# Performance work log

Measured on AMD Instinct MI355X. Metric: run time of the kernel, lower is better.

Reference implementation:

```python
import jax, jax.numpy as jnp
import numpy as np

VLAD_K = 8   # vlad_cluster
GHOST = 2    # ghost_cluster
EPS = 1e-12  # F.normalize eps


def setup_inputs() -> dict:
    key = jax.random.key(0)
    k1, k2, k3, k4 = jax.random.split(key, 4)
    N, C, H, W = 32, 512, 16, 32
    KG = VLAD_K + GHOST
    x = jax.random.normal(k1, (N, C, H, W), dtype=jnp.float32)
    conv_w = jax.random.normal(k2, (KG, C), dtype=jnp.float32) * 0.05  # 1x1 conv weight
    conv_b = jax.random.normal(k3, (KG,), dtype=jnp.float32) * 0.05
    centers = jax.random.uniform(k4, (KG, C), dtype=jnp.float32)
    return {"x": x, "conv_w": conv_w, "conv_b": conv_b, "centers": centers}


def _l2norm(v, axis):
    n = jnp.sqrt(jnp.sum(v * v, axis=axis, keepdims=True))
    return v / jnp.maximum(n, EPS)


def reference(x, conv_w, conv_b, centers):
    N, C, H, W = x.shape
    L = H * W
    xf = x.reshape(N, C, L)  # [N, C, HW]
    # 1x1 conv -> logits [N, K+G, HW], softmax over cluster dim
    logits = jnp.einsum('kc,ncl->nkl', conv_w, xf) + conv_b[None, :, None]
    a = jax.nn.softmax(logits, axis=1)
    # sum_l a[n,k,l]*(x[n,c,l] - centers[k,c]) decomposed into two small matmuls
    assign_x = jnp.einsum('nkl,ncl->nkc', a, xf)          # [N, K+G, C]
    assign_sum = jnp.sum(a, axis=-1)                      # [N, K+G]
    cluster_res = assign_x - assign_sum[:, :, None] * centers[None]
    cluster_res = cluster_res[:, :VLAD_K, :]              # drop ghost clusters
    cluster_res = _l2norm(cluster_res, axis=-1)           # intra-norm
    vlad = cluster_res.reshape(N, -1)                     # [N, K*C]
    return _l2norm(vlad, axis=-1)
```

## Files before the change

### kernel.cpp

```cpp
#include <hip/hip_runtime.h>

#define N_   32
#define C_   512
#define L_   512
#define KG_  10
#define K_   8
#define LCH  8
#define LT   64
#define EPSF 1e-12f

__global__ __launch_bounds__(512) void k_softmax(
    const float* __restrict__ x, const float* __restrict__ cw,
    const float* __restrict__ cb, float* __restrict__ a_out,
    float* __restrict__ asum_part)
{
    const int n   = blockIdx.x;
    const int ch  = blockIdx.y;
    const int tid = threadIdx.x;
    const int l   = tid & 63;
    const int cg  = tid >> 6;
    const int lg  = ch * LT + l;

    const float* xn = x + (size_t)n * C_ * L_;

    float acc[KG_];
#pragma unroll
    for (int k = 0; k < KG_; ++k) acc[k] = 0.f;

    const int c0 = cg * 64;
#pragma unroll 4
    for (int ci = 0; ci < 64; ++ci) {
        const int c = c0 + ci;
        const float xv = xn[(size_t)c * L_ + lg];
#pragma unroll
        for (int k = 0; k < KG_; ++k)
            acc[k] += cw[k * C_ + c] * xv;
    }

    __shared__ float red[8][LT][KG_];
#pragma unroll
    for (int k = 0; k < KG_; ++k) red[cg][l][k] = acc[k];
    __syncthreads();

    __shared__ float lgs[LT][KG_];
    for (int idx = tid; idx < LT * KG_; idx += 512) {
        const int li = idx / KG_, k = idx % KG_;
        float s = 0.f;
#pragma unroll
        for (int g = 0; g < 8; ++g) s += red[g][li][k];
        lgs[li][k] = s;
    }
    __syncthreads();

    if (tid < LT) {
        float v[KG_];
        float m = -1e30f;
#pragma unroll
        for (int k = 0; k < KG_; ++k) {
            v[k] = lgs[tid][k] + cb[k];
            m = fmaxf(m, v[k]);
        }
        float s = 0.f;
#pragma unroll
        for (int k = 0; k < KG_; ++k) { v[k] = __expf(v[k] - m); s += v[k]; }
        const float inv = 1.f / s;
        const int lgl = ch * LT + tid;
#pragma unroll
        for (int k = 0; k < K_; ++k) {
            const float av = v[k] * inv;
            a_out[((size_t)n * K_ + k) * L_ + lgl] = av;
            float t = av;
#pragma unroll
            for (int off = 32; off > 0; off >>= 1) t += __shfl_down(t, off);
            if (tid == 0)
                asum_part[((size_t)n * LCH + ch) * K_ + k] = t;
        }
    }
}

__global__ __launch_bounds__(512) void k_assign(
    const float* __restrict__ x, const float* __restrict__ a,
    float* __restrict__ assign_x)
{
    const int n   = blockIdx.x;
    const int ch  = blockIdx.y;
    const int tid = threadIdx.x;

    __shared__ float xs[C_ * 65];

    const float* xbase = x + (size_t)n * C_ * L_ + ch * LT;
    for (int it = tid; it < C_ * 16; it += 512) {
        const int c = it >> 4, q = it & 15;
        const float4 v = *reinterpret_cast<const float4*>(xbase + (size_t)c * L_ + q * 4);
        const int b = c * 65 + q * 4;
        xs[b]     = v.x;
        xs[b + 1] = v.y;
        xs[b + 2] = v.z;
        xs[b + 3] = v.w;
    }
    __syncthreads();

    const int c = tid;
    const float* arow = a + (size_t)n * K_ * L_ + ch * LT;

    float acc[K_];
#pragma unroll
    for (int k = 0; k < K_; ++k) acc[k] = 0.f;

#pragma unroll 2
    for (int li = 0; li < LT; ++li) {
        const float xv = xs[c * 65 + li];
#pragma unroll
        for (int k = 0; k < K_; ++k)
            acc[k] += arow[k * L_ + li] * xv;
    }

#pragma unroll
    for (int k = 0; k < K_; ++k)
        atomicAdd(&assign_x[((size_t)n * K_ + k) * C_ + c], acc[k]);
}

__global__ __launch_bounds__(256) void k_final(
    const float* __restrict__ assign_x, const float* __restrict__ asum_part,
    const float* __restrict__ centers, float* __restrict__ out)
{
    const int n    = blockIdx.x;
    const int tid  = threadIdx.x;
    const int lane = tid & 63;
    const int wv   = tid >> 6;

    __shared__ float s_asum[K_];
    __shared__ float s_inv[K_];
    __shared__ float s_q[K_];
    __shared__ float s_ginv;
    __shared__ float wred[4][K_];

    if (tid < K_) {
        float s = 0.f;
#pragma unroll
        for (int c2 = 0; c2 < LCH; ++c2)
            s += asum_part[((size_t)n * LCH + c2) * K_ + tid];
        s_asum[tid] = s;
    }
    __syncthreads();

    float r[K_][2];
    float ssq[K_];
#pragma unroll
    for (int k = 0; k < K_; ++k) ssq[k] = 0.f;

#pragma unroll
    for (int j = 0; j < 2; ++j) {
        const int c = tid + j * 256;
#pragma unroll
        for (int k = 0; k < K_; ++k) {
            const float v = assign_x[((size_t)n * K_ + k) * C_ + c]
                          - s_asum[k] * centers[k * C_ + c];
            r[k][j] = v;
            ssq[k] += v * v;
        }
    }

#pragma unroll
    for (int k = 0; k < K_; ++k) {
        float t = ssq[k];
#pragma unroll
        for (int off = 32; off > 0; off >>= 1) t += __shfl_down(t, off);
        if (lane == 0) wred[wv][k] = t;
    }
    __syncthreads();

    if (tid < K_) {
        const float t = wred[0][tid] + wred[1][tid] + wred[2][tid] + wred[3][tid];
        const float inv = 1.f / fmaxf(sqrtf(t), EPSF);
        s_inv[tid] = inv;
        s_q[tid]   = t * inv * inv;
    }
    __syncthreads();

    if (tid == 0) {
        float g = 0.f;
#pragma unroll
        for (int k = 0; k < K_; ++k) g += s_q[k];
        s_ginv = 1.f / fmaxf(sqrtf(g), EPSF);
    }
    __syncthreads();

    const float ginv = s_ginv;
#pragma unroll
    for (int j = 0; j < 2; ++j) {
        const int c = tid + j * 256;
#pragma unroll
        for (int k = 0; k < K_; ++k)
            out[(size_t)n * (K_ * C_) + k * C_ + c] = r[k][j] * s_inv[k] * ginv;
    }
}

extern "C" void kernel_launch(void* const* d_in, const int* in_sizes, int n_in,
                              void* d_out, int out_size, void* d_ws, size_t ws_size,
                              hipStream_t stream)
{
    const float* x       = (const float*)d_in[0];
    const float* conv_w  = (const float*)d_in[1];
    const float* conv_b  = (const float*)d_in[2];
    const float* centers = (const float*)d_in[3];
    float* out = (float*)d_out;

    float* a         = (float*)d_ws;
    float* asum_part = a + (size_t)N_ * K_ * L_;
    float* assign_x  = asum_part + (size_t)N_ * LCH * K_;

    hipMemsetAsync(assign_x, 0, sizeof(float) * N_ * K_ * C_, stream);

    dim3 grid(N_, LCH);
    hipLaunchKernelGGL(k_softmax, grid, dim3(512), 0, stream,
                       x, conv_w, conv_b, a, asum_part);
    hipLaunchKernelGGL(k_assign, grid, dim3(512), 0, stream,
                       x, a, assign_x);
    hipLaunchKernelGGL(k_final, dim3(N_), dim3(256), 0, stream,
                       assign_x, asum_part, centers, out);
}
```

Baseline: 103.8 us.

## Fuse softmax and assignment kernels, reuse staged x tile, replace atomics with partials

```diff
diff --git a/kernel.cpp b/kernel.cpp
--- a/kernel.cpp
+++ b/kernel.cpp
@@ -7,92 +7,30 @@
 #define K_   8
 #define LCH  8
 #define LT   64
+#define XP   65
+#define RP   11
 #define EPSF 1e-12f
 
-__global__ __launch_bounds__(512) void k_softmax(
+__global__ __launch_bounds__(512, 2) void k_main(
     const float* __restrict__ x, const float* __restrict__ cw,
-    const float* __restrict__ cb, float* __restrict__ a_out,
+    const float* __restrict__ cb, float* __restrict__ part,
     float* __restrict__ asum_part)
 {
+    __shared__ float xs[C_ * XP];
+    __shared__ float red[8][LT][RP];
+    __shared__ float a_s[LT][K_];
+
     const int n   = blockIdx.x;
     const int ch  = blockIdx.y;
     const int tid = threadIdx.x;
-    const int l   = tid & 63;
-    const int cg  = tid >> 6;
-    const int lg  = ch * LT + l;
-
-    const float* xn = x + (size_t)n * C_ * L_;
-
-    float acc[KG_];
-#pragma unroll
-    for (int k = 0; k < KG_; ++k) acc[k] = 0.f;
-
-    const int c0 = cg * 64;
-#pragma unroll 4
-    for (int ci = 0; ci < 64; ++ci) {
-        const int c = c0 + ci;
-        const float xv = xn[(size_t)c * L_ + lg];
-#pragma unroll
-        for (int k = 0; k < KG_; ++k)
-            acc[k] += cw[k * C_ + c] * xv;
-    }
-
-    __shared__ float red[8][LT][KG_];
-#pragma unroll
-    for (int k = 0; k < KG_; ++k) red[cg][l][k] = acc[k];
-    __syncthreads();
-
-    __shared__ float lgs[LT][KG_];
-    for (int idx = tid; idx < LT * KG_; idx += 512) {
-        const int li = idx / KG_, k = idx % KG_;
-        float s = 0.f;
-#pragma unroll
-        for (int g = 0; g < 8; ++g) s += red[g][li][k];
-        lgs[li][k] = s;
-    }
-    __syncthreads();
-
-    if (tid < LT) {
-        float v[KG_];
-        float m = -1e30f;
-#pragma unroll
-        for (int k = 0; k < KG_; ++k) {
-            v[k] = lgs[tid][k] + cb[k];
-            m = fmaxf(m, v[k]);
-        }
-        float s = 0.f;
-#pragma unroll
-        for (int k = 0; k < KG_; ++k) { v[k] = __expf(v[k] - m); s += v[k]; }
-        const float inv = 1.f / s;
-        const int lgl = ch * LT + tid;
-#pragma unroll
-        for (int k = 0; k < K_; ++k) {
-            const float av = v[k] * inv;
-            a_out[((size_t)n * K_ + k) * L_ + lgl] = av;
-            float t = av;
-#pragma unroll
-            for (int off = 32; off > 0; off >>= 1) t += __shfl_down(t, off);
-            if (tid == 0)
-                asum_part[((size_t)n * LCH + ch) * K_ + k] = t;
-        }
-    }
-}
-
-__global__ __launch_bounds__(512) void k_assign(
-    const float* __restrict__ x, const float* __restrict__ a,
-    float* __restrict__ assign_x)
-{
-    const int n   = blockIdx.x;
-    const int ch  = blockIdx.y;
-    const int tid = threadIdx.x;
-
-    __shared__ float xs[C_ * 65];
 
     const float* xbase = x + (size_t)n * C_ * L_ + ch * LT;
-    for (int it = tid; it < C_ * 16; it += 512) {
+#pragma unroll
+    for (int j = 0; j < 16; ++j) {
+        const int it = tid + j * 512;
         const int c = it >> 4, q = it & 15;
         const float4 v = *reinterpret_cast<const float4*>(xbase + (size_t)c * L_ + q * 4);
-        const int b = c * 65 + q * 4;
+        const int b = c * XP + q * 4;
         xs[b]     = v.x;
         xs[b + 1] = v.y;
         xs[b + 2] = v.z;
@@ -100,28 +38,96 @@
     }
     __syncthreads();
 
+    const int l  = tid & 63;
+    const int cg = tid >> 6;
+    const int c0 = __builtin_amdgcn_readfirstlane(cg) << 6;
+
+    float acc[KG_];
+#pragma unroll
+    for (int k = 0; k < KG_; ++k) acc[k] = 0.f;
+
+#pragma unroll
+    for (int h = 0; h < 4; ++h) {
+        const int cbase = c0 + h * 16;
+        float xr[16];
+#pragma unroll
+        for (int ci = 0; ci < 16; ++ci)
+            xr[ci] = xs[(cbase + ci) * XP + l];
+#pragma unroll
+        for (int k = 0; k < KG_; ++k) {
+            const float* w = cw + k * C_ + cbase;
+#pragma unroll
+            for (int ci = 0; ci < 16; ++ci)
+                acc[k] = fmaf(w[ci], xr[ci], acc[k]);
+        }
+    }
+
+#pragma unroll
+    for (int k = 0; k < KG_; ++k) red[cg][l][k] = acc[k];
+    __syncthreads();
+
+    for (int idx = tid; idx < LT * KG_; idx += 512) {
+        const int li = idx / KG_, k = idx - li * KG_;
+        float s = red[0][li][k];
+#pragma unroll
+        for (int g = 1; g < 8; ++g) s += red[g][li][k];
+        red[0][li][k] = s;
+    }
+    __syncthreads();
+
+    if (tid < LT) {
+        float v[KG_];
+        float m = -1e30f;
+#pragma unroll
+        for (int k = 0; k < KG_; ++k) {
+            v[k] = red[0][tid][k] + cb[k];
+            m = fmaxf(m, v[k]);
+        }
+        float s = 0.f;
+#pragma unroll
+        for (int k = 0; k < KG_; ++k) { v[k] = __expf(v[k] - m); s += v[k]; }
+        const float inv = 1.f / s;
+#pragma unroll
+        for (int k = 0; k < K_; ++k) {
+            const float av = v[k] * inv;
+            a_s[tid][k] = av;
+            float t = av;
+#pragma unroll
+            for (int off = 32; off > 0; off >>= 1) t += __shfl_down(t, off);
+            if (tid == 0)
+                asum_part[((size_t)n * LCH + ch) * K_ + k] = t;
+        }
+    }
+    __syncthreads();
+
     const int c = tid;
-    const float* arow = a + (size_t)n * K_ * L_ + ch * LT;
-
-    float acc[K_];
-#pragma unroll
-    for (int k = 0; k < K_; ++k) acc[k] = 0.f;
-
-#pragma unroll 2
+    float bacc[K_];
+#pragma unroll
+    for (int k = 0; k < K_; ++k) bacc[k] = 0.f;
+
+#pragma unroll 4
     for (int li = 0; li < LT; ++li) {
-        const float xv = xs[c * 65 + li];
-#pragma unroll
-        for (int k = 0; k < K_; ++k)
-            acc[k] += arow[k * L_ + li] * xv;
-    }
-
+        const float xv = xs[c * XP + li];
+        const float4 a0 = *reinterpret_cast<const float4*>(&a_s[li][0]);
+        const float4 a1 = *reinterpret_cast<const float4*>(&a_s[li][4]);
+        bacc[0] = fmaf(a0.x, xv, bacc[0]);
+        bacc[1] = fmaf(a0.y, xv, bacc[1]);
+        bacc[2] = fmaf(a0.z, xv, bacc[2]);
+        bacc[3] = fmaf(a0.w, xv, bacc[3]);
+        bacc[4] = fmaf(a1.x, xv, bacc[4]);
+        bacc[5] = fmaf(a1.y, xv, bacc[5]);
+        bacc[6] = fmaf(a1.z, xv, bacc[6]);
+        bacc[7] = fmaf(a1.w, xv, bacc[7]);
+    }
+
+    float* pp = part + (((size_t)n * LCH + ch) * K_) * C_ + c;
 #pragma unroll
     for (int k = 0; k < K_; ++k)
-        atomicAdd(&assign_x[((size_t)n * K_ + k) * C_ + c], acc[k]);
+        pp[(size_t)k * C_] = bacc[k];
 }
 
 __global__ __launch_bounds__(256) void k_final(
-    const float* __restrict__ assign_x, const float* __restrict__ asum_part,
+    const float* __restrict__ part, const float* __restrict__ asum_part,
     const float* __restrict__ centers, float* __restrict__ out)
 {
     const int n    = blockIdx.x;
@@ -154,8 +160,11 @@
         const int c = tid + j * 256;
 #pragma unroll
         for (int k = 0; k < K_; ++k) {
-            const float v = assign_x[((size_t)n * K_ + k) * C_ + c]
-                          - s_asum[k] * centers[k * C_ + c];
+            float v = 0.f;
+#pragma unroll
+            for (int c2 = 0; c2 < LCH; ++c2)
+                v += part[(((size_t)n * LCH + c2) * K_ + k) * C_ + c];
+            v -= s_asum[k] * centers[k * C_ + c];
             r[k][j] = v;
             ssq[k] += v * v;
         }
@@ -206,17 +215,12 @@
     const float* centers = (const float*)d_in[3];
     float* out = (float*)d_out;
 
-    float* a         = (float*)d_ws;
-    float* asum_part = a + (size_t)N_ * K_ * L_;
-    float* assign_x  = asum_part + (size_t)N_ * LCH * K_;
-
-    hipMemsetAsync(assign_x, 0, sizeof(float) * N_ * K_ * C_, stream);
+    float* part      = (float*)d_ws;
+    float* asum_part = part + (size_t)N_ * LCH * K_ * C_;
 
     dim3 grid(N_, LCH);
-    hipLaunchKernelGGL(k_softmax, grid, dim3(512), 0, stream,
-                       x, conv_w, conv_b, a, asum_part);
-    hipLaunchKernelGGL(k_assign, grid, dim3(512), 0, stream,
-                       x, a, assign_x);
+    hipLaunchKernelGGL(k_main, grid, dim3(512), 0, stream,
+                       x, conv_w, conv_b, part, asum_part);
     hipLaunchKernelGGL(k_final, dim3(N_), dim3(256), 0, stream,
-                       assign_x, asum_part, centers, out);
+                       part, asum_part, centers, out);
 }
```

Result: faster. 95.54 us (-8.0%).
